# Kernel tuning notes

Measured on AMD Instinct MI355X. Metric: run time of the kernel, lower is better.

Reference implementation:

```python
import jax, jax.numpy as jnp
import numpy as np


def _bilinear_resize(x, out_h, out_w):
    """PyTorch-style bilinear resize, align_corners=False, no antialias. x: [B,C,H,W]."""
    B, C, H, W = x.shape
    sy = H / out_h
    sx = W / out_w
    ys = jnp.maximum((jnp.arange(out_h, dtype=x.dtype) + 0.5) * sy - 0.5, 0.0)
    xs = jnp.maximum((jnp.arange(out_w, dtype=x.dtype) + 0.5) * sx - 0.5, 0.0)
    y0 = jnp.minimum(jnp.floor(ys).astype(jnp.int32), H - 1)
    x0 = jnp.minimum(jnp.floor(xs).astype(jnp.int32), W - 1)
    y1 = jnp.minimum(y0 + 1, H - 1)
    x1 = jnp.minimum(x0 + 1, W - 1)
    ty = ys - y0.astype(x.dtype)  # [out_h]
    tx = xs - x0.astype(x.dtype)  # [out_w]
    row = x[:, :, y0, :] * (1.0 - ty)[None, None, :, None] + x[:, :, y1, :] * ty[None, None, :, None]
    out = row[:, :, :, x0] * (1.0 - tx)[None, None, None, :] + row[:, :, :, x1] * tx[None, None, None, :]
    return out


def setup_inputs() -> dict:
    key = jax.random.key(0)
    ks = jax.random.split(key, 6)
    T, B, Ck, Cv = 4, 4, 128, 512
    H, W, h, w = 64, 64, 32, 32
    return {
        "memory_keys": jax.random.normal(ks[0], (T, B, Ck, H, W), dtype=jnp.float32),
        "memory_values": jax.random.normal(ks[1], (T, B, Cv, H, W), dtype=jnp.float32),
        "query_value": jax.random.normal(ks[2], (B, Cv, H, W), dtype=jnp.float32),
        "memory_keys_low": jax.random.normal(ks[3], (T, B, Ck, h, w), dtype=jnp.float32),
        "memory_values_low": jax.random.normal(ks[4], (T, B, Cv, h, w), dtype=jnp.float32),
        "query_key_low": jax.random.normal(ks[5], (B, Ck, h, w), dtype=jnp.float32),
    }


def reference(memory_keys, memory_values, query_value, memory_keys_low, memory_values_low, query_key_low):
    matmul_norm = False  # init default
    T, B, Ck, h, w = memory_keys_low.shape
    H, W = memory_keys.shape[-2:]
    Cv = memory_values.shape[2]

    # ---- low-level memory read ----
    # memory_keys_low -> [B, Ck, T*h*w]
    mkl = jnp.transpose(memory_keys_low.reshape(T, B, Ck, h * w), (1, 2, 0, 3)).reshape(B, Ck, T * h * w)
    qkl = query_key_low.reshape(B, Ck, h * w)
    # key_attention: [B, T*h*w, h*w]
    key_attention = jnp.einsum('bkm,bkq->bmq', mkl, qkl)
    if matmul_norm:
        key_attention = key_attention * (Ck ** -0.5)
    key_attention = jax.nn.softmax(key_attention, axis=1)
    mvl = jnp.transpose(memory_values_low.reshape(T, B, Cv, h * w), (1, 2, 0, 3)).reshape(B, Cv, T * h * w)
    memory = jnp.einsum('bvm,bmq->bvq', mvl, key_attention).reshape(B, Cv, h, w)

    # ---- high-level channel attention ----
    g_keys = jnp.transpose(memory_keys, (1, 0, 2, 3, 4)).reshape(B, T, Ck, H * W)
    g_vals = jnp.transpose(memory_values, (1, 0, 2, 3, 4)).reshape(B, T, Cv, H * W)
    # g_attn: [B, T, Ck, Cv] = keys @ values^T over spatial dim
    g_attn = jnp.einsum('btkp,btvp->btkv', g_keys, g_vals)
    if matmul_norm:
        g_attn = g_attn * (Cv ** -0.5)
    g_attn = jax.nn.softmax(g_attn, axis=1)  # softmax over the T (frame) axis

    qv = query_value.reshape(B, Cv, H * W)
    # [B, T, Ck, H*W] -> [B, T*Ck, H, W]
    qv_out = jnp.einsum('btkv,bvq->btkq', g_attn, qv).reshape(B, T * Ck, H, W)
    qv_out = _bilinear_resize(qv_out, h, w)

    return jnp.concatenate([qv_out, memory], axis=1)  # [B, T*Ck+Cv, h, w]
```

## Files before the change

### kernel.cpp

```cpp
#include <hip/hip_runtime.h>

#define T_ 4
#define B_ 4
#define CK 128
#define CV 512
#define PP 4096
#define QQ 1024
#define MM 4096
#define NS 8

using f32x2  = __attribute__((ext_vector_type(2))) float;
using f32x4  = __attribute__((ext_vector_type(4))) float;
using bf16   = __bf16;
using bf16x2 = __attribute__((ext_vector_type(2))) __bf16;
using bf16x4 = __attribute__((ext_vector_type(4))) __bf16;
using bf16x8 = __attribute__((ext_vector_type(8))) __bf16;
using f16    = _Float16;
using f16x8  = __attribute__((ext_vector_type(8))) _Float16;

__device__ __forceinline__ f32x4 mfma16(bf16x8 a, bf16x8 b, f32x4 c) {
    return __builtin_amdgcn_mfma_f32_16x16x32_bf16(a, b, c, 0, 0, 0);
}
__device__ __forceinline__ f32x4 mfma16h(f16x8 a, f16x8 b, f32x4 c) {
    return __builtin_amdgcn_mfma_f32_16x16x32_f16(a, b, c, 0, 0, 0);
}

__device__ __forceinline__ void gload16(const void* g, void* l) {
    __builtin_amdgcn_global_load_lds(
        (const __attribute__((address_space(1))) void*)g,
        (__attribute__((address_space(3))) void*)l, 16, 0, 0);
}

__global__ __launch_bounds__(256) void k_stage1(
        const float* __restrict__ mkl, const float* __restrict__ qkl,
        bf16* __restrict__ Pt, float* __restrict__ cs_part,
        const float* __restrict__ mvl, bf16* __restrict__ Ab,
        const float* __restrict__ qv,  float* __restrict__ qvp,
        const float* __restrict__ mk,  f16* __restrict__ mkh,
        const float* __restrict__ mv,  f16* __restrict__ mvh) {
    __shared__ __align__(16) char smem[34816];
    const int bid = blockIdx.x;
    const int tid = threadIdx.x;

    if (bid < 1024) {
        bf16* As = (bf16*)smem;
        bf16* Bs = (bf16*)(smem + 10240);
        bf16* Ts = (bf16*)smem;

        int sw  = (bid & 7) * 128 + (bid >> 3);
        const int b  = sw >> 8;
        const int r  = sw & 255;
        const int qy = r >> 5;
        const int mx = r & 31;
        const int m0 = mx * 128;
        const int q0 = qy * 128;
        const int t  = m0 >> 10;
        const int sm0 = m0 & 1023;

        const int lane = tid & 63;
        const int wid  = tid >> 6;
        const int wr = wid >> 1, wc = wid & 1;
        const int g = lane >> 4, li = lane & 15;

        const float* Abase = mkl + (((size_t)(t * B_ + b) * CK) << 10) + sm0;
        const float* Bbase = qkl + (((size_t)b * CK) << 10) + q0;
        const int ml   = tid & 127;
        const int half = tid >> 7;

        const f32x4 fz = {0.f, 0.f, 0.f, 0.f};
        f32x4 acc[4][4];
#pragma unroll
        for (int i = 0; i < 4; ++i)
#pragma unroll
            for (int j = 0; j < 4; ++j) acc[i][j] = fz;

        for (int k0 = 0; k0 < CK; k0 += 32) {
#pragma unroll
            for (int j = 0; j < 8; ++j) {
                int kk = 4 * j + 2 * half;
                float a0 = Abase[(k0 + kk) * 1024 + ml];
                float a1 = Abase[(k0 + kk + 1) * 1024 + ml];
                bf16x2 pa; pa.x = (bf16)a0; pa.y = (bf16)a1;
                *(bf16x2*)(As + ml * 40 + kk) = pa;
                float b0 = Bbase[(k0 + kk) * 1024 + ml];
                float b1 = Bbase[(k0 + kk + 1) * 1024 + ml];
                bf16x2 pb; pb.x = (bf16)b0; pb.y = (bf16)b1;
                *(bf16x2*)(Bs + ml * 40 + kk) = pb;
            }
            __syncthreads();
            bf16x8 af[4], bfr[4];
#pragma unroll
            for (int mf = 0; mf < 4; ++mf)
                af[mf] = *(const bf16x8*)(As + (wr * 64 + mf * 16 + li) * 40 + g * 8);
#pragma unroll
            for (int nf = 0; nf < 4; ++nf)
                bfr[nf] = *(const bf16x8*)(Bs + (wc * 64 + nf * 16 + li) * 40 + g * 8);
#pragma unroll
            for (int mf = 0; mf < 4; ++mf)
#pragma unroll
                for (int nf = 0; nf < 4; ++nf)
                    acc[mf][nf] = mfma16(af[mf], bfr[nf], acc[mf][nf]);
            __syncthreads();
        }

        float cs[4] = {0.f, 0.f, 0.f, 0.f};
#pragma unroll
        for (int mf = 0; mf < 4; ++mf)
#pragma unroll
            for (int nf = 0; nf < 4; ++nf) {
                f32x4 v = acc[mf][nf];
                float e0 = __expf(v.x), e1 = __expf(v.y);
                float e2 = __expf(v.z), e3 = __expf(v.w);
                cs[nf] += e0 + e1 + e2 + e3;
                bf16x4 e; e.x = (bf16)e0; e.y = (bf16)e1; e.z = (bf16)e2; e.w = (bf16)e3;
                int col  = wc * 64 + nf * 16 + li;
                int rowb = wr * 64 + mf * 16 + g * 4;
                *(bf16x4*)(Ts + col * 136 + rowb) = e;
            }
#pragma unroll
        for (int nf = 0; nf < 4; ++nf) {
            float s = cs[nf];
            s += __shfl_xor(s, 16);
            s += __shfl_xor(s, 32);
            if (g == 0)
                cs_part[(size_t)(((b * 32 + mx) * 2 + wr) << 10) + q0 + wc * 64 + nf * 16 + li] = s;
        }
        __syncthreads();
#pragma unroll
        for (int pass = 0; pass < 8; ++pass) {
            int idx = pass * 256 + tid;
            int row = idx >> 4;
            int ch  = (idx & 15) * 8;
            bf16x8 v = *(const bf16x8*)(Ts + row * 136 + ch);
            *(bf16x8*)(Pt + (size_t)(b * QQ + q0 + row) * MM + m0 + ch) = v;
        }
    } else if (bid < 2048) {
        int base = (bid - 1024) * 4096 + tid;
#pragma unroll
        for (int i = 0; i < 16; ++i) {
            int idx = base + i * 256;
            f32x4 a = __builtin_nontemporal_load((const f32x4*)mv + (size_t)idx * 2);
            f32x4 c = __builtin_nontemporal_load((const f32x4*)mv + (size_t)idx * 2 + 1);
            f16x8 o;
            o[0] = (f16)a.x; o[1] = (f16)a.y; o[2] = (f16)a.z; o[3] = (f16)a.w;
            o[4] = (f16)c.x; o[5] = (f16)c.y; o[6] = (f16)c.z; o[7] = (f16)c.w;
            ((f16x8*)mvh)[idx] = o;
        }
    } else if (bid < 2304) {
        int base = (bid - 2048) * 4096 + tid;
#pragma unroll
        for (int i = 0; i < 16; ++i) {
            int idx = base + i * 256;
            f32x4 a = __builtin_nontemporal_load((const f32x4*)mk + (size_t)idx * 2);
            f32x4 c = __builtin_nontemporal_load((const f32x4*)mk + (size_t)idx * 2 + 1);
            f16x8 o;
            o[0] = (f16)a.x; o[1] = (f16)a.y; o[2] = (f16)a.z; o[3] = (f16)a.w;
            o[4] = (f16)c.x; o[5] = (f16)c.y; o[6] = (f16)c.z; o[7] = (f16)c.w;
            ((f16x8*)mkh)[idx] = o;
        }
    } else if (bid < 2560) {
        int base = (bid - 2304) * 4096 + tid;
#pragma unroll
        for (int i = 0; i < 16; ++i) {
            int idx = base + i * 256;
            f32x4 a = __builtin_nontemporal_load((const f32x4*)mvl + (size_t)idx * 2);
            f32x4 c = __builtin_nontemporal_load((const f32x4*)mvl + (size_t)idx * 2 + 1);
            bf16x8 o;
            o[0] = (bf16)a.x; o[1] = (bf16)a.y; o[2] = (bf16)a.z; o[3] = (bf16)a.w;
            o[4] = (bf16)c.x; o[5] = (bf16)c.y; o[6] = (bf16)c.z; o[7] = (bf16)c.w;
            ((bf16x8*)Ab)[idx] = o;
        }
    } else {
        int base = (bid - 2560) * 4096 + tid;
#pragma unroll
        for (int i = 0; i < 16; ++i) {
            int idx = base + i * 256;
            int q  = idx & (QQ - 1);
            int bv = idx >> 10;
            int y = q >> 5, x = q & 31;
            const float* src = qv + ((size_t)bv << 12);
            f32x2 r0 = __builtin_nontemporal_load((const f32x2*)(src + y * 128 + 2 * x));
            f32x2 r1 = __builtin_nontemporal_load((const f32x2*)(src + y * 128 + 64 + 2 * x));
            qvp[idx] = 0.25f * (r0.x + r0.y + r1.x + r1.y);
        }
    }
}

__global__ __launch_bounds__(256, 2) void k_stage2(
        const f16* __restrict__ mkh, const f16* __restrict__ mvh,
        float* __restrict__ Gp,
        const bf16* __restrict__ Ab, const bf16* __restrict__ Pt,
        float* __restrict__ Mp,
        const float* __restrict__ cs_part, float* __restrict__ colsum) {
    __shared__ __align__(16) char smem[65536];
    const int bid = blockIdx.x;
    const int tid = threadIdx.x;

    if (bid < 512) {
        f16* lsA = (f16*)smem;
        f16* lsB = (f16*)(smem + 32768);

        int sw  = (bid & 7) * 64 + (bid >> 3);
        const int bt = sw >> 5;
        const int rx = sw & 31;
        const int ks = rx >> 2;
        const int v0 = (rx & 3) * 128;
        const int b = bt >> 2, t = bt & 3;

        const int lane = tid & 63;
        const int w    = tid >> 6;
        const int wr = w >> 1, wc = w & 1;
        const int g = lane >> 4, li = lane & 15;
        const int rr = lane >> 3;
        const int cg = (lane & 7) ^ rr;

        const f16* Abase = mkh + ((size_t)(t * B_ + b) * CK) * PP + ks * 512;
        const f16* Bbase = mvh + ((size_t)((t * B_ + b) * CV + v0)) * PP + ks * 512;

        auto STAGE = [&](int buf, int j) {
            int mg = j * 64;
#pragma unroll
            for (int cc = 0; cc < 4; ++cc) {
                int c = cc * 4 + w;
                int r = c * 8 + rr;
                gload16(Abase + (size_t)r * PP + mg + cg * 8, lsA + buf * 8192 + c * 512);
                gload16(Bbase + (size_t)r * PP + mg + cg * 8, lsB + buf * 8192 + c * 512);
            }
        };
        auto FRAG = [&](const f16* base, int r, int G) -> f16x8 {
            int x = r & 7;
            return *(const f16x8*)(base + (r >> 3) * 512 + x * 64 + ((G ^ x) * 8));
        };

        const f32x4 fz = {0.f, 0.f, 0.f, 0.f};
        f32x4 acc[4][4];
#pragma unroll
        for (int i = 0; i < 4; ++i)
#pragma unroll
            for (int j = 0; j < 4; ++j) acc[i][j] = fz;

        STAGE(0, 0);
        __syncthreads();
        int cur = 0;

        for (int j = 0; j < 8; ++j) {
            if (j + 1 < 8) STAGE(cur ^ 1, j + 1);
#pragma unroll
            for (int kc = 0; kc < 2; ++kc) {
                f16x8 af[4], bfr[4];
#pragma unroll
                for (int mf = 0; mf < 4; ++mf)
                    af[mf] = FRAG(lsA + cur * 8192, wr * 64 + mf * 16 + li, kc * 4 + g);
#pragma unroll
                for (int nf = 0; nf < 4; ++nf)
                    bfr[nf] = FRAG(lsB + cur * 8192, wc * 64 + nf * 16 + li, kc * 4 + g);
#pragma unroll
                for (int mf = 0; mf < 4; ++mf)
#pragma unroll
                    for (int nf = 0; nf < 4; ++nf)
                        acc[mf][nf] = mfma16h(af[mf], bfr[nf], acc[mf][nf]);
            }
            __syncthreads();
            cur ^= 1;
        }

        float* outp = Gp + (size_t)(ks * 16 + bt) * CK * CV + v0;
#pragma unroll
        for (int mf = 0; mf < 4; ++mf)
#pragma unroll
            for (int nf = 0; nf < 4; ++nf) {
                int k = wr * 64 + mf * 16 + g * 4;
                int v = wc * 64 + nf * 16 + li;
                f32x4 a = acc[mf][nf];
                outp[(size_t)(k + 0) * CV + v] = a.x;
                outp[(size_t)(k + 1) * CV + v] = a.y;
                outp[(size_t)(k + 2) * CV + v] = a.z;
                outp[(size_t)(k + 3) * CV + v] = a.w;
            }
    } else if (bid < 1024) {
        bf16* lsA = (bf16*)smem;
        bf16* lsB = (bf16*)(smem + 32768);

        int mb = bid - 512;
        int sw  = (mb & 7) * 64 + (mb >> 3);
        const int bt = sw >> 5;
        const int rx = sw & 31;
        const int q0 = (rx >> 2) * 128;
        const int v0 = (rx & 3) * 128;
        const int b = bt >> 2, t = bt & 3;

        const int lane = tid & 63;
        const int w    = tid >> 6;
        const int wr = w >> 1, wc = w & 1;
        const int g = lane >> 4, li = lane & 15;
        const int rr = lane >> 3;
        const int cg = (lane & 7) ^ rr;

        const bf16* Abase = Ab + (((size_t)((t * B_ + b) * CV + v0)) << 10);
        const bf16* Bbase = Pt + (size_t)(b * QQ + q0) * MM + t * 1024;

        auto STAGE = [&](int buf, int j) {
            int mg = j * 64;
#pragma unroll
            for (int cc = 0; cc < 4; ++cc) {
                int c = cc * 4 + w;
                int r = c * 8 + rr;
                gload16(Abase + (size_t)r * 1024 + mg + cg * 8, lsA + buf * 8192 + c * 512);
                gload16(Bbase + (size_t)r * MM   + mg + cg * 8, lsB + buf * 8192 + c * 512);
            }
        };
        auto FRAG = [&](const bf16* base, int r, int G) -> bf16x8 {
            int x = r & 7;
            return *(const bf16x8*)(base + (r >> 3) * 512 + x * 64 + ((G ^ x) * 8));
        };

        const f32x4 fz = {0.f, 0.f, 0.f, 0.f};
        f32x4 acc[4][4];
#pragma unroll
        for (int i = 0; i < 4; ++i)
#pragma unroll
            for (int j = 0; j < 4; ++j) acc[i][j] = fz;

        STAGE(0, 0);
        __syncthreads();
        int cur = 0;

        for (int j = 0; j < 16; ++j) {
            if (j + 1 < 16) STAGE(cur ^ 1, j + 1);
#pragma unroll
            for (int kc = 0; kc < 2; ++kc) {
                bf16x8 af[4], bfr[4];
#pragma unroll
                for (int mf = 0; mf < 4; ++mf)
                    af[mf] = FRAG(lsA + cur * 8192, wr * 64 + mf * 16 + li, kc * 4 + g);
#pragma unroll
                for (int nf = 0; nf < 4; ++nf)
                    bfr[nf] = FRAG(lsB + cur * 8192, wc * 64 + nf * 16 + li, kc * 4 + g);
#pragma unroll
                for (int mf = 0; mf < 4; ++mf)
#pragma unroll
                    for (int nf = 0; nf < 4; ++nf)
                        acc[mf][nf] = mfma16(af[mf], bfr[nf], acc[mf][nf]);
            }
            __syncthreads();
            cur ^= 1;
        }

#pragma unroll
        for (int nf = 0; nf < 4; ++nf) {
            int q = q0 + wc * 64 + nf * 16 + li;
#pragma unroll
            for (int mf = 0; mf < 4; ++mf) {
                int v = v0 + wr * 64 + mf * 16 + g * 4;
                f32x4 a = acc[mf][nf];
                float* base = Mp + (((size_t)bt * CV + v) << 10) + q;
                base[0 << 10] = a.x;
                base[1 << 10] = a.y;
                base[2 << 10] = a.z;
                base[3 << 10] = a.w;
            }
        }
    } else {
        int idx = (bid - 1024) * 256 + tid;
        int q = idx & (QQ - 1);
        int b = idx >> 10;
        float s = 0.f;
#pragma unroll 8
        for (int r = 0; r < 64; ++r)
            s += cs_part[(size_t)(((b * 64 + r)) << 10) + q];
        colsum[idx] = s;
    }
}

__global__ __launch_bounds__(256) void k_stage3(
        const float* __restrict__ Gp, bf16* __restrict__ Wt,
        const float* __restrict__ Mp, const float* __restrict__ colsum,
        float* __restrict__ out) {
    const int bid = blockIdx.x;
    const int tid = threadIdx.x;

    if (bid < 1024) {
        int idx = bid * 256 + tid;
        int v = idx & (CV - 1);
        int bk = idx >> 9;
        int k = bk & (CK - 1);
        int b = bk >> 7;
        float gv[4];
#pragma unroll
        for (int t = 0; t < 4; ++t) {
            float s = 0.f;
#pragma unroll
            for (int ks = 0; ks < NS; ++ks)
                s += Gp[((size_t)(ks * 16 + b * 4 + t) * CK + k) * CV + v];
            gv[t] = s;
        }
        float mx = fmaxf(fmaxf(gv[0], gv[1]), fmaxf(gv[2], gv[3]));
        float e[4], sum = 0.f;
#pragma unroll
        for (int t = 0; t < 4; ++t) { e[t] = __expf(gv[t] - mx); sum += e[t]; }
        float inv = 1.f / sum;
#pragma unroll
        for (int t = 0; t < 4; ++t)
            Wt[((size_t)((b * 4 + t) * CK + k)) * CV + v] = (bf16)(e[t] * inv);
    } else {
        int idx = ((bid - 1024) * 256 + tid) * 4;
        int q = idx & (QQ - 1);
        int v = (idx >> 10) & (CV - 1);
        int b = idx >> 19;
        f32x4 s = {0.f, 0.f, 0.f, 0.f};
#pragma unroll
        for (int t = 0; t < 4; ++t) {
            f32x4 m = *(const f32x4*)(Mp + (((size_t)((b * 4 + t) * CV + v)) << 10) + q);
            s.x += m.x; s.y += m.y; s.z += m.z; s.w += m.w;
        }
        f32x4 cs = *(const f32x4*)(colsum + (b << 10) + q);
        f32x4 o;
        o.x = s.x / cs.x; o.y = s.y / cs.y; o.z = s.z / cs.z; o.w = s.w / cs.w;
        *(f32x4*)(out + (((size_t)(b * 1024 + 512 + v)) << 10) + q) = o;
    }
}

__global__ __launch_bounds__(256) void k_qvout(const bf16* __restrict__ Wt,
                                               const float* __restrict__ QVp,
                                               float* __restrict__ out) {
    __shared__ __align__(16) char smem[27648];
    bf16* As = (bf16*)smem;
    bf16* Bs = (bf16*)(smem + 18432);

    int bid = blockIdx.x;
    int sw  = (bid & 7) * 32 + (bid >> 3);
    const int bt = sw >> 4;
    const int q0 = (sw & 15) * 64;
    const int b = bt >> 2, t = bt & 3;

    const int tid = threadIdx.x;
    const int lane = tid & 63;
    const int wid = tid >> 6;
    const int wr = wid >> 1, wc = wid & 1;
    const int g = lane >> 4, li = lane & 15;

    const bf16*  Abase = Wt + (size_t)bt * CK * CV;
    const float* Bbase = QVp + (((size_t)b * CV) << 10) + q0;

    const f32x4 fz = {0.f, 0.f, 0.f, 0.f};
    f32x4 acc[4][2];
#pragma unroll
    for (int i = 0; i < 4; ++i)
#pragma unroll
        for (int j = 0; j < 2; ++j) acc[i][j] = fz;

    const int ql  = tid & 63;
    const int grp = tid >> 6;

    for (int kk = 0; kk < 8; ++kk) {
        int vk0 = kk * 64;
#pragma unroll
        for (int pass = 0; pass < 4; ++pass) {
            int idx = pass * 256 + tid;
            int row = idx >> 3;
            int ch  = (idx & 7) * 8;
            bf16x8 v = *(const bf16x8*)(Abase + (size_t)row * CV + vk0 + ch);
            *(bf16x8*)(As + row * 72 + ch) = v;
        }
#pragma unroll
        for (int j = 0; j < 8; ++j) {
            int vv = 2 * grp + 8 * j;
            float b0 = Bbase[(size_t)(vk0 + vv) * 1024 + ql];
            float b1 = Bbase[(size_t)(vk0 + vv + 1) * 1024 + ql];
            bf16x2 p; p.x = (bf16)b0; p.y = (bf16)b1;
            *(bf16x2*)(Bs + ql * 72 + vv) = p;
        }
        __syncthreads();
#pragma unroll
        for (int kc = 0; kc < 2; ++kc) {
            bf16x8 af[4], bfr[2];
#pragma unroll
            for (int mf = 0; mf < 4; ++mf)
                af[mf] = *(const bf16x8*)(As + (wr * 64 + mf * 16 + li) * 72 + kc * 32 + g * 8);
#pragma unroll
            for (int nf = 0; nf < 2; ++nf)
                bfr[nf] = *(const bf16x8*)(Bs + (wc * 32 + nf * 16 + li) * 72 + kc * 32 + g * 8);
#pragma unroll
            for (int mf = 0; mf < 4; ++mf)
#pragma unroll
                for (int nf = 0; nf < 2; ++nf)
                    acc[mf][nf] = mfma16(af[mf], bfr[nf], acc[mf][nf]);
        }
        __syncthreads();
    }

#pragma unroll
    for (int mf = 0; mf < 4; ++mf)
#pragma unroll
        for (int nf = 0; nf < 2; ++nf) {
            int k = wr * 64 + mf * 16 + g * 4;
            int q = q0 + wc * 32 + nf * 16 + li;
            f32x4 a = acc[mf][nf];
            size_t base = ((size_t)(b * 1024 + t * 128 + k) << 10) + q;
            out[base]             = a.x;
            out[base + (1 << 10)] = a.y;
            out[base + (2 << 10)] = a.z;
            out[base + (3 << 10)] = a.w;
        }
}

extern "C" void kernel_launch(void* const* d_in, const int* in_sizes, int n_in,
                              void* d_out, int out_size, void* d_ws, size_t ws_size,
                              hipStream_t stream) {
    (void)in_sizes; (void)n_in; (void)out_size; (void)ws_size;
    const float* mk  = (const float*)d_in[0];
    const float* mv  = (const float*)d_in[1];
    const float* qv  = (const float*)d_in[2];
    const float* mkl = (const float*)d_in[3];
    const float* mvl = (const float*)d_in[4];
    const float* qkl = (const float*)d_in[5];
    float* out = (float*)d_out;

    char* w = (char*)d_ws;
    bf16*  Pt      = (bf16*)w;  w += (size_t)B_ * QQ * MM * 2;
    float* QVp     = (float*)w; w += (size_t)B_ * CV * QQ * 4;
    float* Gp      = (float*)w; w += (size_t)NS * 16 * CK * CV * 4;
    bf16*  Wt      = (bf16*)w;  w += (size_t)B_ * T_ * CK * CV * 2;
    float* colsum  = (float*)w; w += (size_t)B_ * QQ * 4;
    bf16*  Ab      = (bf16*)w;  w += (size_t)T_ * B_ * CV * QQ * 2;
    float* cs_part = (float*)w; w += (size_t)B_ * 64 * QQ * 4;
    float* Mp      = (float*)w; w += (size_t)T_ * B_ * CV * QQ * 4;
    f16*   mkh     = (f16*)w;   w += (size_t)T_ * B_ * CK * PP * 2;
    f16*   mvh     = (f16*)w;   w += (size_t)T_ * B_ * CV * PP * 2;

    k_stage1<<<dim3(3072), 256, 0, stream>>>(mkl, qkl, Pt, cs_part,
                                             mvl, Ab, qv, QVp,
                                             mk, mkh, mv, mvh);
    k_stage2<<<dim3(1040), 256, 0, stream>>>(mkh, mvh, Gp, Ab, Pt, Mp,
                                             cs_part, colsum);
    k_stage3<<<dim3(3072), 256, 0, stream>>>(Gp, Wt, Mp, colsum, out);
    k_qvout <<<dim3(256),  256, 0, stream>>>(Wt, QVp, out);
}
```

Before: 162.0 us.

## Interleave GEMM and conversion blocks in stage1 and halve transpose LDS

Stage1 blocks are reassigned so every third block runs the exp-GEMM tile and the rest run the fp32-to-half conversion work. Compute-bound and bandwidth-bound blocks therefore share the GPU at the same time instead of running in separate phases. The transpose staging buffer is cut to half size by writing the exp tile in two passes, each storing one 64-row half. This shrinks shared memory from 34 KB to 20 KB to allow more resident blocks, at the cost of extra barriers and 16 held bf16x4 registers per thread.

```diff
diff --git a/kernel.cpp b/kernel.cpp
--- a/kernel.cpp
+++ b/kernel.cpp
@@ -38,16 +38,17 @@
         const float* __restrict__ qv,  float* __restrict__ qvp,
         const float* __restrict__ mk,  f16* __restrict__ mkh,
         const float* __restrict__ mv,  f16* __restrict__ mvh) {
-    __shared__ __align__(16) char smem[34816];
+    __shared__ __align__(16) char smem[20480];
     const int bid = blockIdx.x;
     const int tid = threadIdx.x;
 
-    if (bid < 1024) {
+    if (bid % 3 == 0) {
         bf16* As = (bf16*)smem;
         bf16* Bs = (bf16*)(smem + 10240);
-        bf16* Ts = (bf16*)smem;
-
-        int sw  = (bid & 7) * 128 + (bid >> 3);
+        bf16* Th = (bf16*)smem;
+
+        int lb  = bid / 3;
+        int sw  = (lb & 7) * 128 + (lb >> 3);
         const int b  = sw >> 8;
         const int r  = sw & 255;
         const int qy = r >> 5;
@@ -104,6 +105,7 @@
         }
 
         float cs[4] = {0.f, 0.f, 0.f, 0.f};
+        bf16x4 ebuf[4][4];
 #pragma unroll
         for (int mf = 0; mf < 4; ++mf)
 #pragma unroll
@@ -113,9 +115,7 @@
                 float e2 = __expf(v.z), e3 = __expf(v.w);
                 cs[nf] += e0 + e1 + e2 + e3;
                 bf16x4 e; e.x = (bf16)e0; e.y = (bf16)e1; e.z = (bf16)e2; e.w = (bf16)e3;
-                int col  = wc * 64 + nf * 16 + li;
-                int rowb = wr * 64 + mf * 16 + g * 4;
-                *(bf16x4*)(Ts + col * 136 + rowb) = e;
+                ebuf[mf][nf] = e;
             }
 #pragma unroll
         for (int nf = 0; nf < 4; ++nf) {
@@ -125,63 +125,80 @@
             if (g == 0)
                 cs_part[(size_t)(((b * 32 + mx) * 2 + wr) << 10) + q0 + wc * 64 + nf * 16 + li] = s;
         }
-        __syncthreads();
-#pragma unroll
-        for (int pass = 0; pass < 8; ++pass) {
-            int idx = pass * 256 + tid;
-            int row = idx >> 4;
-            int ch  = (idx & 15) * 8;
-            bf16x8 v = *(const bf16x8*)(Ts + row * 136 + ch);
-            *(bf16x8*)(Pt + (size_t)(b * QQ + q0 + row) * MM + m0 + ch) = v;
-        }
-    } else if (bid < 2048) {
-        int base = (bid - 1024) * 4096 + tid;
-#pragma unroll
-        for (int i = 0; i < 16; ++i) {
-            int idx = base + i * 256;
-            f32x4 a = __builtin_nontemporal_load((const f32x4*)mv + (size_t)idx * 2);
-            f32x4 c = __builtin_nontemporal_load((const f32x4*)mv + (size_t)idx * 2 + 1);
-            f16x8 o;
-            o[0] = (f16)a.x; o[1] = (f16)a.y; o[2] = (f16)a.z; o[3] = (f16)a.w;
-            o[4] = (f16)c.x; o[5] = (f16)c.y; o[6] = (f16)c.z; o[7] = (f16)c.w;
-            ((f16x8*)mvh)[idx] = o;
-        }
-    } else if (bid < 2304) {
-        int base = (bid - 2048) * 4096 + tid;
-#pragma unroll
-        for (int i = 0; i < 16; ++i) {
-            int idx = base + i * 256;
-            f32x4 a = __builtin_nontemporal_load((const f32x4*)mk + (size_t)idx * 2);
-            f32x4 c = __builtin_nontemporal_load((const f32x4*)mk + (size_t)idx * 2 + 1);
-            f16x8 o;
-            o[0] = (f16)a.x; o[1] = (f16)a.y; o[2] = (f16)a.z; o[3] = (f16)a.w;
-            o[4] = (f16)c.x; o[5] = (f16)c.y; o[6] = (f16)c.z; o[7] = (f16)c.w;
-            ((f16x8*)mkh)[idx] = o;
-        }
-    } else if (bid < 2560) {
-        int base = (bid - 2304) * 4096 + tid;
-#pragma unroll
-        for (int i = 0; i < 16; ++i) {
-            int idx = base + i * 256;
-            f32x4 a = __builtin_nontemporal_load((const f32x4*)mvl + (size_t)idx * 2);
-            f32x4 c = __builtin_nontemporal_load((const f32x4*)mvl + (size_t)idx * 2 + 1);
-            bf16x8 o;
-            o[0] = (bf16)a.x; o[1] = (bf16)a.y; o[2] = (bf16)a.z; o[3] = (bf16)a.w;
-            o[4] = (bf16)c.x; o[5] = (bf16)c.y; o[6] = (bf16)c.z; o[7] = (bf16)c.w;
-            ((bf16x8*)Ab)[idx] = o;
+#pragma unroll
+        for (int p = 0; p < 2; ++p) {
+            __syncthreads();
+            if (wr == p) {
+#pragma unroll
+                for (int mf = 0; mf < 4; ++mf)
+#pragma unroll
+                    for (int nf = 0; nf < 4; ++nf) {
+                        int col  = wc * 64 + nf * 16 + li;
+                        int rowb = mf * 16 + g * 4;
+                        *(bf16x4*)(Th + col * 72 + rowb) = ebuf[mf][nf];
+                    }
+            }
+            __syncthreads();
+#pragma unroll
+            for (int pass = 0; pass < 4; ++pass) {
+                int idx = pass * 256 + tid;
+                int row = idx >> 3;
+                int ch  = (idx & 7) * 8;
+                bf16x8 v = *(const bf16x8*)(Th + row * 72 + ch);
+                *(bf16x8*)(Pt + (size_t)(b * QQ + q0 + row) * MM + m0 + p * 64 + ch) = v;
+            }
         }
     } else {
-        int base = (bid - 2560) * 4096 + tid;
-#pragma unroll
-        for (int i = 0; i < 16; ++i) {
-            int idx = base + i * 256;
-            int q  = idx & (QQ - 1);
-            int bv = idx >> 10;
-            int y = q >> 5, x = q & 31;
-            const float* src = qv + ((size_t)bv << 12);
-            f32x2 r0 = __builtin_nontemporal_load((const f32x2*)(src + y * 128 + 2 * x));
-            f32x2 r1 = __builtin_nontemporal_load((const f32x2*)(src + y * 128 + 64 + 2 * x));
-            qvp[idx] = 0.25f * (r0.x + r0.y + r1.x + r1.y);
+        int sid = bid - bid / 3 - 1;
+        if (sid < 1024) {
+            int base = sid * 4096 + tid;
+#pragma unroll
+            for (int i = 0; i < 16; ++i) {
+                int idx = base + i * 256;
+                f32x4 a = __builtin_nontemporal_load((const f32x4*)mv + (size_t)idx * 2);
+                f32x4 c = __builtin_nontemporal_load((const f32x4*)mv + (size_t)idx * 2 + 1);
+                f16x8 o;
+                o[0] = (f16)a.x; o[1] = (f16)a.y; o[2] = (f16)a.z; o[3] = (f16)a.w;
+                o[4] = (f16)c.x; o[5] = (f16)c.y; o[6] = (f16)c.z; o[7] = (f16)c.w;
+                ((f16x8*)mvh)[idx] = o;
+            }
+        } else if (sid < 1280) {
+            int base = (sid - 1024) * 4096 + tid;
+#pragma unroll
+            for (int i = 0; i < 16; ++i) {
+                int idx = base + i * 256;
+                f32x4 a = __builtin_nontemporal_load((const f32x4*)mk + (size_t)idx * 2);
+                f32x4 c = __builtin_nontemporal_load((const f32x4*)mk + (size_t)idx * 2 + 1);
+                f16x8 o;
+                o[0] = (f16)a.x; o[1] = (f16)a.y; o[2] = (f16)a.z; o[3] = (f16)a.w;
+                o[4] = (f16)c.x; o[5] = (f16)c.y; o[6] = (f16)c.z; o[7] = (f16)c.w;
+                ((f16x8*)mkh)[idx] = o;
+            }
+        } else if (sid < 1536) {
+            int base = (sid - 1280) * 4096 + tid;
+#pragma unroll
+            for (int i = 0; i < 16; ++i) {
+                int idx = base + i * 256;
+                f32x4 a = __builtin_nontemporal_load((const f32x4*)mvl + (size_t)idx * 2);
+                f32x4 c = __builtin_nontemporal_load((const f32x4*)mvl + (size_t)idx * 2 + 1);
+                bf16x8 o;
+                o[0] = (bf16)a.x; o[1] = (bf16)a.y; o[2] = (bf16)a.z; o[3] = (bf16)a.w;
+                o[4] = (bf16)c.x; o[5] = (bf16)c.y; o[6] = (bf16)c.z; o[7] = (bf16)c.w;
+                ((bf16x8*)Ab)[idx] = o;
+            }
+        } else {
+            int base = (sid - 1536) * 4096 + tid;
+#pragma unroll
+            for (int i = 0; i < 16; ++i) {
+                int idx = base + i * 256;
+                int q  = idx & (QQ - 1);
+                int bv = idx >> 10;
+                int y = q >> 5, x = q & 31;
+                const float* src = qv + ((size_t)bv << 12);
+                f32x2 r0 = __builtin_nontemporal_load((const f32x2*)(src + y * 128 + 2 * x));
+                f32x2 r1 = __builtin_nontemporal_load((const f32x2*)(src + y * 128 + 64 + 2 * x));
+                qvp[idx] = 0.25f * (r0.x + r0.y + r1.x + r1.y);
+            }
         }
     }
 }
```

Result: faster. 137.5 us (-15.2%).
